# Kernel optimization log

Hardware: AMD Instinct MI355X
Metric: run time of the kernel (lower is better)

## Reference

```python
import jax, jax.numpy as jnp
import numpy as np

NS, NV = 16, 4            # multiplicities of 0e and 1o in in/out irreps
N_NODES, N_EDGES = 50000, 800000
INV_SQRT3 = 1.0 / np.sqrt(3.0).astype(np.float32)  # CG norm for 1o x 1o -> 0e
INV_SQRT2 = 1.0 / np.sqrt(2.0).astype(np.float32)  # 2 paths per output irrep
INV_SQRT_NS = 1.0 / np.sqrt(float(NS))
INV_SQRT_NV = 1.0 / np.sqrt(float(NV))


def setup_inputs() -> dict:
    key = jax.random.key(0)
    ks = jax.random.split(key, 8)
    node_attr = jax.random.normal(ks[0], (N_NODES, NS + 3 * NV), dtype=jnp.float32)
    edge_attr = jax.random.normal(ks[1], (N_EDGES, 64), dtype=jnp.float32)
    edge_sh = jax.random.normal(ks[2], (N_EDGES, 4), dtype=jnp.float32)
    edge_index = jax.random.randint(ks[3], (2, N_EDGES), 0, N_NODES, dtype=jnp.int32)
    n_weights = NS * NS + NV * NS + NS * NV + NV * NV  # 400
    W1 = jax.random.normal(ks[4], (64, 64), dtype=jnp.float32) / np.sqrt(64.0)
    b1 = jnp.zeros((64,), jnp.float32)
    W2 = jax.random.normal(ks[5], (64, n_weights), dtype=jnp.float32) / np.sqrt(64.0)
    b2 = jnp.zeros((n_weights,), jnp.float32)
    return {"node_attr": node_attr, "edge_attr": edge_attr, "edge_sh": edge_sh,
            "edge_index": edge_index, "W1": W1, "b1": b1, "W2": W2, "b2": b2}


def reference(node_attr, edge_attr, edge_sh, edge_index, W1, b1, W2, b2):
    E = edge_attr.shape[0]
    N = node_attr.shape[0]
    edge_src, edge_dst = edge_index[0], edge_index[1]

    # per-edge tensor-product weights from the MLP (dropout disabled at inference)
    h = jax.nn.relu(edge_attr @ W1 + b1)
    dense = h @ W2 + b2  # [E, 400]
    i0 = NS * NS
    i1 = i0 + NV * NS
    i2 = i1 + NS * NV
    w_ss = dense[:, :i0].reshape(E, NS, NS)   # 0e x 0e -> 0e
    w_vs = dense[:, i0:i1].reshape(E, NV, NS)  # 1o x 1o -> 0e
    w_sv = dense[:, i1:i2].reshape(E, NS, NV)  # 0e x 1o -> 1o
    w_vv = dense[:, i2:].reshape(E, NV, NV)    # 1o x 0e -> 1o

    # gather destination-node features per edge
    x = node_attr[edge_dst]            # [E, 28]
    x_s = x[:, :NS]                    # [E, NS]   scalars
    x_v = x[:, NS:].reshape(E, NV, 3)  # [E, NV,3] vectors
    sh_s = edge_sh[:, 0:1]             # [E, 1]
    sh_v = edge_sh[:, 1:4]             # [E, 3]

    # scalar outputs: two parity-allowed CG paths
    dot_vv = jnp.einsum('evd,ed->ev', x_v, sh_v) * INV_SQRT3  # 1o x 1o -> 0e
    out_s = (jnp.einsum('ei,eio->eo', x_s * sh_s, w_ss) * INV_SQRT_NS
             + jnp.einsum('ev,evo->eo', dot_vv, w_vs) * INV_SQRT_NV) * INV_SQRT2

    # vector outputs: two parity-allowed CG paths
    out_v = (jnp.einsum('ei,eio,ed->eod', x_s, w_sv, sh_v) * INV_SQRT_NS
             + jnp.einsum('evd,evo->eod', x_v * sh_s[:, :, None], w_vv) * INV_SQRT_NV) * INV_SQRT2

    out_e = jnp.concatenate([out_s, out_v.reshape(E, 3 * NV)], axis=-1)  # [E, 28]

    # scatter-mean onto source nodes
    summed = jax.ops.segment_sum(out_e, edge_src, num_segments=N)
    cnt = jax.ops.segment_sum(jnp.ones((E,), out_e.dtype), edge_src, num_segments=N)
    out = summed / jnp.maximum(cnt, 1.0)[:, None]

    # residual (out dim == in dim, so pad width is zero)
    return out + node_attr
```

## Files before the change

kernel.cpp:

```cpp
#include <hip/hip_runtime.h>

#define EDGES 800000
#define NODES 50000
#define CH 28
#define NWT 400
#define SCAN_NB 196
#define FIXS 65536.0f
#define FIXR (1.0f/65536.0f)

typedef __attribute__((ext_vector_type(8))) short bf16x8;
typedef __attribute__((ext_vector_type(4))) float f32x4;

#define WAVE_FENCE() __builtin_amdgcn_sched_barrier(0)

__device__ __forceinline__ short f2bf(float f) {
    union { float f; unsigned u; } v; v.f = f;
    unsigned r = v.u + 0x7FFFu + ((v.u >> 16) & 1u);
    return (short)(r >> 16);
}

#define SWZ(b, row) ((b) ^ (((row) & 7) << 4))

__global__ __launch_bounds__(256) void hist_kernel(const int* __restrict__ eidx,
                                                   int* __restrict__ counts) {
    int e = blockIdx.x * 256 + threadIdx.x;
    if (e < EDGES) atomicAdd(&counts[eidx[e]], 1);
}

__global__ __launch_bounds__(256) void scan1_kernel(const int* __restrict__ counts,
                                                    int* __restrict__ offsets,
                                                    int* __restrict__ bsum) {
    __shared__ int tmp[256];
    int t = threadIdx.x;
    int i = blockIdx.x * 256 + t;
    int v = (i < NODES) ? counts[i] : 0;
    tmp[t] = v;
    __syncthreads();
    int x = v;
    for (int d = 1; d < 256; d <<= 1) {
        int y = (t >= d) ? tmp[t - d] : 0;
        __syncthreads();
        x += y; tmp[t] = x;
        __syncthreads();
    }
    if (i < NODES) offsets[i] = x - v;
    if (t == 255) bsum[blockIdx.x] = x;
}

__global__ __launch_bounds__(256) void scan2_kernel(int* __restrict__ bsum) {
    __shared__ int tmp[256];
    int t = threadIdx.x;
    int v = (t < SCAN_NB) ? bsum[t] : 0;
    tmp[t] = v;
    __syncthreads();
    int x = v;
    for (int d = 1; d < 256; d <<= 1) {
        int y = (t >= d) ? tmp[t - d] : 0;
        __syncthreads();
        x += y; tmp[t] = x;
        __syncthreads();
    }
    if (t < SCAN_NB) bsum[t] = x - v;
}

__global__ __launch_bounds__(256) void scan3_kernel(int* __restrict__ offsets,
                                                    const int* __restrict__ bsum) {
    int i = blockIdx.x * 256 + threadIdx.x;
    if (i < NODES) offsets[i] += bsum[blockIdx.x];
}

__global__ __launch_bounds__(256) void perm_kernel(const int* __restrict__ eidx,
                                                   const int* __restrict__ offsets,
                                                   int* __restrict__ cursor,
                                                   int* __restrict__ perm) {
    int e = blockIdx.x * 256 + threadIdx.x;
    if (e < EDGES) {
        int s = eidx[e];
        int pos = offsets[s] + atomicAdd(&cursor[s], 1);
        perm[pos] = e;
    }
}

__global__ __launch_bounds__(256, 2) void tpconv_kernel(
    const float* __restrict__ node_attr,
    const float* __restrict__ edge_attr,
    const float* __restrict__ edge_sh,
    const int*   __restrict__ eidx,
    const float* __restrict__ W1,
    const float* __restrict__ b1,
    const float* __restrict__ W2,
    const float* __restrict__ b2,
    int* __restrict__ outq,
    const int* __restrict__ perm)
{
    __shared__ __align__(16) short w2t[NWT * 64];
    __shared__ float b2s[NWT];
    __shared__ __align__(16) short hbuf[4][16 * 64];
    __shared__ float edata[4][16 * 53];
    __shared__ int   srcb[4][16];
    __shared__ int   eids[4][16];

    const int tid  = threadIdx.x;
    const int lane = tid & 63;
    const int wid  = tid >> 6;
    const int cl   = lane & 15;
    const int qd   = lane >> 4;

    for (int f = tid; f < NWT * 64; f += 256) {
        int n = f >> 6, j = f & 63;
        int byte = SWZ(n * 128 + j * 2, n);
        w2t[byte >> 1] = f2bf(W2[j * NWT + n]);
    }
    for (int f = tid; f < NWT; f += 256) b2s[f] = b2[f];

    float b1v[4];
    bf16x8 w1f[2][4];
    #pragma unroll
    for (int nt = 0; nt < 4; ++nt) {
        b1v[nt] = b1[nt * 16 + cl];
        #pragma unroll
        for (int ks = 0; ks < 2; ++ks) {
            bf16x8 fr;
            #pragma unroll
            for (int i = 0; i < 8; ++i) {
                int k = ks * 32 + qd * 8 + i;
                fr[i] = f2bf(W1[k * 64 + nt * 16 + cl]);
            }
            w1f[ks][nt] = fr;
        }
    }
    __syncthreads();

    const float INV3 = 0.57735026919f;
    const float CS_  = 0.17677669529f;
    const float CV_  = 0.35355339059f;

    const int tiles = EDGES / 16;
    for (int tile = blockIdx.x * 4 + wid; tile < tiles; tile += gridDim.x * 4) {
        const int ebase = tile * 16;

        if (lane < 16) {
            const int slot = ebase + lane;
            const int e  = perm[slot];
            const int s  = eidx[e];
            const int dn = eidx[EDGES + e];
            srcb[wid][lane] = s;
            eids[wid][lane] = e;
            const float4 sh4 = *reinterpret_cast<const float4*>(edge_sh + (size_t)e * 4);
            float xs[16], xv[12];
            {
                const float4* xp = reinterpret_cast<const float4*>(node_attr + (size_t)dn * CH);
                float4 q0 = xp[0], q1 = xp[1], q2 = xp[2], q3 = xp[3], q4 = xp[4], q5 = xp[5], q6 = xp[6];
                xs[0]=q0.x; xs[1]=q0.y; xs[2]=q0.z; xs[3]=q0.w;
                xs[4]=q1.x; xs[5]=q1.y; xs[6]=q1.z; xs[7]=q1.w;
                xs[8]=q2.x; xs[9]=q2.y; xs[10]=q2.z; xs[11]=q2.w;
                xs[12]=q3.x; xs[13]=q3.y; xs[14]=q3.z; xs[15]=q3.w;
                xv[0]=q4.x; xv[1]=q4.y; xv[2]=q4.z; xv[3]=q4.w;
                xv[4]=q5.x; xv[5]=q5.y; xv[6]=q5.z; xv[7]=q5.w;
                xv[8]=q6.x; xv[9]=q6.y; xv[10]=q6.z; xv[11]=q6.w;
            }
            const float shs = sh4.x, sv0 = sh4.y, sv1 = sh4.z, sv2 = sh4.w;
            float* ed = &edata[wid][lane * 53];
            #pragma unroll
            for (int i = 0; i < 16; ++i) {
                ed[i]      = xs[i] * shs * CS_;
                ed[20 + i] = xs[i] * CS_;
            }
            #pragma unroll
            for (int v = 0; v < 4; ++v) {
                float dot = (xv[3*v] * sv0 + xv[3*v+1] * sv1 + xv[3*v+2] * sv2) * INV3;
                ed[16 + v] = dot * CV_;
                ed[36 + 3*v + 0] = xv[3*v + 0] * shs * CV_;
                ed[36 + 3*v + 1] = xv[3*v + 1] * shs * CV_;
                ed[36 + 3*v + 2] = xv[3*v + 2] * shs * CV_;
            }
            ed[48] = sv0; ed[49] = sv1; ed[50] = sv2;
        }
        WAVE_FENCE();

        const int es = eids[wid][cl];
        const float4* ap = reinterpret_cast<const float4*>(edge_attr + (size_t)es * 64);
        float4 a0 = ap[qd*2], a1 = ap[qd*2 + 1], a2 = ap[8 + qd*2], a3 = ap[8 + qd*2 + 1];
        bf16x8 af0, af1;
        af0[0]=f2bf(a0.x); af0[1]=f2bf(a0.y); af0[2]=f2bf(a0.z); af0[3]=f2bf(a0.w);
        af0[4]=f2bf(a1.x); af0[5]=f2bf(a1.y); af0[6]=f2bf(a1.z); af0[7]=f2bf(a1.w);
        af1[0]=f2bf(a2.x); af1[1]=f2bf(a2.y); af1[2]=f2bf(a2.z); af1[3]=f2bf(a2.w);
        af1[4]=f2bf(a3.x); af1[5]=f2bf(a3.y); af1[6]=f2bf(a3.z); af1[7]=f2bf(a3.w);

        short* hb = hbuf[wid];
        #pragma unroll
        for (int nt = 0; nt < 4; ++nt) {
            f32x4 acc = { b1v[nt], b1v[nt], b1v[nt], b1v[nt] };
            acc = __builtin_amdgcn_mfma_f32_16x16x32_bf16(af0, w1f[0][nt], acc, 0, 0, 0);
            acc = __builtin_amdgcn_mfma_f32_16x16x32_bf16(af1, w1f[1][nt], acc, 0, 0, 0);
            #pragma unroll
            for (int r = 0; r < 4; ++r) {
                int m = qd * 4 + r;
                float hv = fmaxf(acc[r], 0.0f);
                int byte = SWZ(m * 128 + (nt * 16 + cl) * 2, m);
                hb[byte >> 1] = f2bf(hv);
            }
        }
        WAVE_FENCE();

        bf16x8 h0 = *reinterpret_cast<bf16x8*>(reinterpret_cast<char*>(hb) + SWZ(cl * 128 + qd * 16, cl));
        bf16x8 h1 = *reinterpret_cast<bf16x8*>(reinterpret_cast<char*>(hb) + SWZ(cl * 128 + 64 + qd * 16, cl));
        WAVE_FENCE();

        f32x4 outs = {0.f, 0.f, 0.f, 0.f};
        f32x4 pacc = {0.f, 0.f, 0.f, 0.f};
        float qacc[4][3] = {{0,0,0},{0,0,0},{0,0,0},{0,0,0}};
        const float* edw = edata[wid];
        const char* wb = reinterpret_cast<const char*>(w2t);
        #pragma unroll
        for (int ct = 0; ct < 25; ++ct) {
            int n = ct * 16 + cl;
            bf16x8 bf0 = *reinterpret_cast<const bf16x8*>(wb + SWZ(n * 128 + qd * 16, n));
            bf16x8 bf1 = *reinterpret_cast<const bf16x8*>(wb + SWZ(n * 128 + 64 + qd * 16, n));
            float bb = b2s[n];
            f32x4 t = { bb, bb, bb, bb };
            t = __builtin_amdgcn_mfma_f32_16x16x32_bf16(h0, bf0, t, 0, 0, 0);
            t = __builtin_amdgcn_mfma_f32_16x16x32_bf16(h1, bf1, t, 0, 0, 0);
            if (ct < 16) {
                #pragma unroll
                for (int r = 0; r < 4; ++r)
                    outs[r] += edw[(qd*4 + r) * 53 + ct] * t[r];
            } else if (ct < 20) {
                #pragma unroll
                for (int r = 0; r < 4; ++r)
                    outs[r] += edw[(qd*4 + r) * 53 + 16 + (ct - 16)] * t[r];
            } else if (ct < 24) {
                int il = cl >> 2;
                #pragma unroll
                for (int r = 0; r < 4; ++r)
                    pacc[r] += edw[(qd*4 + r) * 53 + 20 + 4*(ct - 20) + il] * t[r];
            } else {
                int v = cl >> 2;
                #pragma unroll
                for (int r = 0; r < 4; ++r) {
                    #pragma unroll
                    for (int d = 0; d < 3; ++d)
                        qacc[r][d] += edw[(qd*4 + r) * 53 + 36 + 3*v + d] * t[r];
                }
            }
        }

        #pragma unroll
        for (int r = 0; r < 4; ++r) {
            float p = pacc[r];
            p += __shfl_xor(p, 4);
            p += __shfl_xor(p, 8);
            pacc[r] = p;
            #pragma unroll
            for (int d = 0; d < 3; ++d) {
                float q = qacc[r][d];
                q += __shfl_xor(q, 4);
                q += __shfl_xor(q, 8);
                qacc[r][d] = q;
            }
        }

        float* stf = reinterpret_cast<float*>(hb);
        #pragma unroll
        for (int r = 0; r < 4; ++r)
            stf[(qd*4 + r) * CH + cl] = outs[r];
        if (cl < 12) {
            int o = cl & 3, d = cl >> 2;
            #pragma unroll
            for (int r = 0; r < 4; ++r) {
                int m = qd * 4 + r;
                float qv = (d == 0) ? qacc[r][0] : ((d == 1) ? qacc[r][1] : qacc[r][2]);
                stf[m * CH + 16 + o * 3 + d] = edw[m * 53 + 48 + d] * pacc[r] + qv;
            }
        }
        WAVE_FENCE();

        if (lane < CH) {
            int cur = srcb[wid][0];
            float acc2 = 0.0f;
            for (int m = 0; m < 16; ++m) {
                int s = srcb[wid][m];
                if (s != cur) {
                    atomicAdd(&outq[(size_t)cur * CH + lane], (int)rintf(acc2 * FIXS));
                    acc2 = 0.0f; cur = s;
                }
                acc2 += stf[m * CH + lane];
            }
            atomicAdd(&outq[(size_t)cur * CH + lane], (int)rintf(acc2 * FIXS));
        }
        WAVE_FENCE();
    }
}

__global__ __launch_bounds__(256) void finalize_kernel(int* __restrict__ outq,
                                                       const int* __restrict__ counts,
                                                       const float* __restrict__ node_attr) {
    int idx = blockIdx.x * 256 + threadIdx.x;
    if (idx < NODES * CH) {
        int n = idx / CH;
        int q = outq[idx];
        float r = ((float)q * FIXR) / fmaxf((float)counts[n], 1.0f) + node_attr[idx];
        outq[idx] = __float_as_int(r);
    }
}

extern "C" void kernel_launch(void* const* d_in, const int* in_sizes, int n_in,
                              void* d_out, int out_size, void* d_ws, size_t ws_size,
                              hipStream_t stream) {
    const float* node_attr = (const float*)d_in[0];
    const float* edge_attr = (const float*)d_in[1];
    const float* edge_sh   = (const float*)d_in[2];
    const int*   eidx      = (const int*)d_in[3];
    const float* W1 = (const float*)d_in[4];
    const float* b1 = (const float*)d_in[5];
    const float* W2 = (const float*)d_in[6];
    const float* b2 = (const float*)d_in[7];

    const size_t OFF_OFFSETS = 204800;
    const size_t OFF_CURSOR  = 409600;
    const size_t OFF_BSUM    = 614400;
    const size_t OFF_PERM    = 616448;

    int* counts  = (int*)d_ws;
    int* offsets = (int*)((char*)d_ws + OFF_OFFSETS);
    int* cursor  = (int*)((char*)d_ws + OFF_CURSOR);
    int* bsum    = (int*)((char*)d_ws + OFF_BSUM);
    int* perm    = (int*)((char*)d_ws + OFF_PERM);

    const int EB = (EDGES + 255) / 256;

    hipMemsetAsync(counts, 0, NODES * sizeof(int), stream);
    hipMemsetAsync(cursor, 0, NODES * sizeof(int), stream);
    hipMemsetAsync(d_out, 0, (size_t)NODES * CH * sizeof(float), stream);

    hist_kernel<<<EB, 256, 0, stream>>>(eidx, counts);
    scan1_kernel<<<SCAN_NB, 256, 0, stream>>>(counts, offsets, bsum);
    scan2_kernel<<<1, 256, 0, stream>>>(bsum);
    scan3_kernel<<<SCAN_NB, 256, 0, stream>>>(offsets, bsum);
    perm_kernel<<<EB, 256, 0, stream>>>(eidx, offsets, cursor, perm);

    tpconv_kernel<<<512, 256, 0, stream>>>(node_attr, edge_attr, edge_sh, eidx,
                                           W1, b1, W2, b2, (int*)d_out, perm);
    finalize_kernel<<<(NODES * CH + 255) / 256, 256, 0, stream>>>((int*)d_out, counts, node_attr);
}
```

Measured before the change: 272.2 us.

## Software-pipeline per-tile gathers with register prefetch of next tile

Restructures the persistent tile loop so each wave prefetches the next tile's edge ids, edge_attr, edge_sh and node features into registers while it computes the current tile, and loads the perm index two tiles ahead. The node feature gather is split across 32 lanes instead of 16, and the shared eids buffer is removed. The aim is to hide global gather latency behind MFMA work, at the cost of more live registers under the 2-blocks-per-SM launch bound.

```diff
diff --git a/kernel.cpp b/kernel.cpp
--- a/kernel.cpp
+++ b/kernel.cpp
@@ -17,6 +17,13 @@
     union { float f; unsigned u; } v; v.f = f;
     unsigned r = v.u + 0x7FFFu + ((v.u >> 16) & 1u);
     return (short)(r >> 16);
+}
+
+__device__ __forceinline__ bf16x8 pack8(float4 u, float4 v) {
+    bf16x8 h;
+    h[0] = f2bf(u.x); h[1] = f2bf(u.y); h[2] = f2bf(u.z); h[3] = f2bf(u.w);
+    h[4] = f2bf(v.x); h[5] = f2bf(v.y); h[6] = f2bf(v.z); h[7] = f2bf(v.w);
+    return h;
 }
 
 #define SWZ(b, row) ((b) ^ (((row) & 7) << 4))
@@ -80,6 +87,13 @@
         perm[pos] = e;
     }
 }
+
+struct TileRegs {
+    float4 a0, a1, a2, a3;
+    float4 sh;
+    float4 x0, x1, x2, x3;
+    int es, src;
+};
 
 __global__ __launch_bounds__(256, 2) void tpconv_kernel(
     const float* __restrict__ node_attr,
@@ -98,7 +112,6 @@
     __shared__ __align__(16) short hbuf[4][16 * 64];
     __shared__ float edata[4][16 * 53];
     __shared__ int   srcb[4][16];
-    __shared__ int   eids[4][16];
 
     const int tid  = threadIdx.x;
     const int lane = tid & 63;
@@ -135,73 +148,101 @@
     const float CS_  = 0.17677669529f;
     const float CV_  = 0.35355339059f;
 
-    const int tiles = EDGES / 16;
-    for (int tile = blockIdx.x * 4 + wid; tile < tiles; tile += gridDim.x * 4) {
-        const int ebase = tile * 16;
-
-        if (lane < 16) {
-            const int slot = ebase + lane;
-            const int e  = perm[slot];
-            const int s  = eidx[e];
-            const int dn = eidx[EDGES + e];
-            srcb[wid][lane] = s;
-            eids[wid][lane] = e;
-            const float4 sh4 = *reinterpret_cast<const float4*>(edge_sh + (size_t)e * 4);
-            float xs[16], xv[12];
-            {
-                const float4* xp = reinterpret_cast<const float4*>(node_attr + (size_t)dn * CH);
-                float4 q0 = xp[0], q1 = xp[1], q2 = xp[2], q3 = xp[3], q4 = xp[4], q5 = xp[5], q6 = xp[6];
-                xs[0]=q0.x; xs[1]=q0.y; xs[2]=q0.z; xs[3]=q0.w;
-                xs[4]=q1.x; xs[5]=q1.y; xs[6]=q1.z; xs[7]=q1.w;
-                xs[8]=q2.x; xs[9]=q2.y; xs[10]=q2.z; xs[11]=q2.w;
-                xs[12]=q3.x; xs[13]=q3.y; xs[14]=q3.z; xs[15]=q3.w;
-                xv[0]=q4.x; xv[1]=q4.y; xv[2]=q4.z; xv[3]=q4.w;
-                xv[4]=q5.x; xv[5]=q5.y; xv[6]=q5.z; xv[7]=q5.w;
-                xv[8]=q6.x; xv[9]=q6.y; xv[10]=q6.z; xv[11]=q6.w;
-            }
-            const float shs = sh4.x, sv0 = sh4.y, sv1 = sh4.z, sv2 = sh4.w;
-            float* ed = &edata[wid][lane * 53];
+    const int tiles  = EDGES / 16;
+    const int STRIDE = gridDim.x << 2;
+    const int w0     = blockIdx.x * 4 + wid;
+
+    short* hb  = hbuf[wid];
+    float* edwv = edata[wid];
+    const char* wb = reinterpret_cast<const char*>(w2t);
+
+    TileRegs C, N;
+    {
+        int slot = w0 * 16 + cl;
+        C.es  = perm[slot];
+        C.src = eidx[C.es];
+        int dst = eidx[EDGES + C.es];
+        const float4* ap = reinterpret_cast<const float4*>(edge_attr + (size_t)C.es * 64);
+        C.a0 = ap[qd*2]; C.a1 = ap[qd*2+1]; C.a2 = ap[8+qd*2]; C.a3 = ap[8+qd*2+1];
+        C.sh = *reinterpret_cast<const float4*>(edge_sh + (size_t)C.es * 4);
+        if (lane < 32) {
+            const float4* xp = reinterpret_cast<const float4*>(node_attr + (size_t)dst * CH);
+            if (lane < 16) { C.x0 = xp[0]; C.x1 = xp[1]; C.x2 = xp[2]; C.x3 = xp[3]; }
+            else           { C.x0 = xp[4]; C.x1 = xp[5]; C.x2 = xp[6]; }
+        }
+        int t1 = w0 + STRIDE;
+        int slot1 = (t1 < tiles) ? t1 * 16 + cl : cl;
+        N.es = perm[slot1];
+    }
+
+    for (int t = w0; t < tiles; t += STRIDE) {
+        int t2 = t + 2 * STRIDE;
+        int slot2 = (t2 < tiles) ? t2 * 16 + cl : cl;
+        int esF = perm[slot2];
+
+        N.src = eidx[N.es];
+        int ndst = eidx[EDGES + N.es];
+        {
+            const float4* ap = reinterpret_cast<const float4*>(edge_attr + (size_t)N.es * 64);
+            N.a0 = ap[qd*2]; N.a1 = ap[qd*2+1]; N.a2 = ap[8+qd*2]; N.a3 = ap[8+qd*2+1];
+            N.sh = *reinterpret_cast<const float4*>(edge_sh + (size_t)N.es * 4);
+        }
+
+        {
+            const float shs = C.sh.x, sv0 = C.sh.y, sv1 = C.sh.z, sv2 = C.sh.w;
+            float* ed = &edwv[cl * 53];
+            if (lane < 16) {
+                srcb[wid][cl] = C.src;
+                float xs[16] = { C.x0.x, C.x0.y, C.x0.z, C.x0.w,
+                                 C.x1.x, C.x1.y, C.x1.z, C.x1.w,
+                                 C.x2.x, C.x2.y, C.x2.z, C.x2.w,
+                                 C.x3.x, C.x3.y, C.x3.z, C.x3.w };
+                #pragma unroll
+                for (int i = 0; i < 16; ++i) {
+                    ed[i]      = xs[i] * shs * CS_;
+                    ed[20 + i] = xs[i] * CS_;
+                }
+            } else if (lane < 32) {
+                float xv[12] = { C.x0.x, C.x0.y, C.x0.z, C.x0.w,
+                                 C.x1.x, C.x1.y, C.x1.z, C.x1.w,
+                                 C.x2.x, C.x2.y, C.x2.z, C.x2.w };
+                #pragma unroll
+                for (int v = 0; v < 4; ++v) {
+                    float dot = (xv[3*v] * sv0 + xv[3*v+1] * sv1 + xv[3*v+2] * sv2) * INV3;
+                    ed[16 + v] = dot * CV_;
+                    ed[36 + 3*v + 0] = xv[3*v + 0] * shs * CV_;
+                    ed[36 + 3*v + 1] = xv[3*v + 1] * shs * CV_;
+                    ed[36 + 3*v + 2] = xv[3*v + 2] * shs * CV_;
+                }
+                ed[48] = sv0; ed[49] = sv1; ed[50] = sv2;
+            }
+        }
+        WAVE_FENCE();
+
+        {
+            bf16x8 af0 = pack8(C.a0, C.a1);
+            bf16x8 af1 = pack8(C.a2, C.a3);
             #pragma unroll
-            for (int i = 0; i < 16; ++i) {
-                ed[i]      = xs[i] * shs * CS_;
-                ed[20 + i] = xs[i] * CS_;
-            }
-            #pragma unroll
-            for (int v = 0; v < 4; ++v) {
-                float dot = (xv[3*v] * sv0 + xv[3*v+1] * sv1 + xv[3*v+2] * sv2) * INV3;
-                ed[16 + v] = dot * CV_;
-                ed[36 + 3*v + 0] = xv[3*v + 0] * shs * CV_;
-                ed[36 + 3*v + 1] = xv[3*v + 1] * shs * CV_;
-                ed[36 + 3*v + 2] = xv[3*v + 2] * shs * CV_;
-            }
-            ed[48] = sv0; ed[49] = sv1; ed[50] = sv2;
-        }
-        WAVE_FENCE();
-
-        const int es = eids[wid][cl];
-        const float4* ap = reinterpret_cast<const float4*>(edge_attr + (size_t)es * 64);
-        float4 a0 = ap[qd*2], a1 = ap[qd*2 + 1], a2 = ap[8 + qd*2], a3 = ap[8 + qd*2 + 1];
-        bf16x8 af0, af1;
-        af0[0]=f2bf(a0.x); af0[1]=f2bf(a0.y); af0[2]=f2bf(a0.z); af0[3]=f2bf(a0.w);
-        af0[4]=f2bf(a1.x); af0[5]=f2bf(a1.y); af0[6]=f2bf(a1.z); af0[7]=f2bf(a1.w);
-        af1[0]=f2bf(a2.x); af1[1]=f2bf(a2.y); af1[2]=f2bf(a2.z); af1[3]=f2bf(a2.w);
-        af1[4]=f2bf(a3.x); af1[5]=f2bf(a3.y); af1[6]=f2bf(a3.z); af1[7]=f2bf(a3.w);
-
-        short* hb = hbuf[wid];
-        #pragma unroll
-        for (int nt = 0; nt < 4; ++nt) {
-            f32x4 acc = { b1v[nt], b1v[nt], b1v[nt], b1v[nt] };
-            acc = __builtin_amdgcn_mfma_f32_16x16x32_bf16(af0, w1f[0][nt], acc, 0, 0, 0);
-            acc = __builtin_amdgcn_mfma_f32_16x16x32_bf16(af1, w1f[1][nt], acc, 0, 0, 0);
-            #pragma unroll
-            for (int r = 0; r < 4; ++r) {
-                int m = qd * 4 + r;
-                float hv = fmaxf(acc[r], 0.0f);
-                int byte = SWZ(m * 128 + (nt * 16 + cl) * 2, m);
-                hb[byte >> 1] = f2bf(hv);
-            }
-        }
-        WAVE_FENCE();
+            for (int nt = 0; nt < 4; ++nt) {
+                f32x4 acc = { b1v[nt], b1v[nt], b1v[nt], b1v[nt] };
+                acc = __builtin_amdgcn_mfma_f32_16x16x32_bf16(af0, w1f[0][nt], acc, 0, 0, 0);
+                acc = __builtin_amdgcn_mfma_f32_16x16x32_bf16(af1, w1f[1][nt], acc, 0, 0, 0);
+                #pragma unroll
+                for (int r = 0; r < 4; ++r) {
+                    int m = qd * 4 + r;
+                    float hv = fmaxf(acc[r], 0.0f);
+                    int byte = SWZ(m * 128 + (nt * 16 + cl) * 2, m);
+                    hb[byte >> 1] = f2bf(hv);
+                }
+            }
+        }
+        WAVE_FENCE();
+
+        if (lane < 32) {
+            const float4* xp = reinterpret_cast<const float4*>(node_attr + (size_t)ndst * CH);
+            if (lane < 16) { N.x0 = xp[0]; N.x1 = xp[1]; N.x2 = xp[2]; N.x3 = xp[3]; }
+            else           { N.x0 = xp[4]; N.x1 = xp[5]; N.x2 = xp[6]; }
+        }
 
         bf16x8 h0 = *reinterpret_cast<bf16x8*>(reinterpret_cast<char*>(hb) + SWZ(cl * 128 + qd * 16, cl));
         bf16x8 h1 = *reinterpret_cast<bf16x8*>(reinterpret_cast<char*>(hb) + SWZ(cl * 128 + 64 + qd * 16, cl));
@@ -210,37 +251,36 @@
         f32x4 outs = {0.f, 0.f, 0.f, 0.f};
         f32x4 pacc = {0.f, 0.f, 0.f, 0.f};
         float qacc[4][3] = {{0,0,0},{0,0,0},{0,0,0},{0,0,0}};
-        const float* edw = edata[wid];
-        const char* wb = reinterpret_cast<const char*>(w2t);
+        const float* edw = edwv;
         #pragma unroll
         for (int ct = 0; ct < 25; ++ct) {
             int n = ct * 16 + cl;
             bf16x8 bf0 = *reinterpret_cast<const bf16x8*>(wb + SWZ(n * 128 + qd * 16, n));
             bf16x8 bf1 = *reinterpret_cast<const bf16x8*>(wb + SWZ(n * 128 + 64 + qd * 16, n));
             float bb = b2s[n];
-            f32x4 t = { bb, bb, bb, bb };
-            t = __builtin_amdgcn_mfma_f32_16x16x32_bf16(h0, bf0, t, 0, 0, 0);
-            t = __builtin_amdgcn_mfma_f32_16x16x32_bf16(h1, bf1, t, 0, 0, 0);
+            f32x4 tt = { bb, bb, bb, bb };
+            tt = __builtin_amdgcn_mfma_f32_16x16x32_bf16(h0, bf0, tt, 0, 0, 0);
+            tt = __builtin_amdgcn_mfma_f32_16x16x32_bf16(h1, bf1, tt, 0, 0, 0);
             if (ct < 16) {
                 #pragma unroll
                 for (int r = 0; r < 4; ++r)
-                    outs[r] += edw[(qd*4 + r) * 53 + ct] * t[r];
+                    outs[r] += edw[(qd*4 + r) * 53 + ct] * tt[r];
             } else if (ct < 20) {
                 #pragma unroll
                 for (int r = 0; r < 4; ++r)
-                    outs[r] += edw[(qd*4 + r) * 53 + 16 + (ct - 16)] * t[r];
+                    outs[r] += edw[(qd*4 + r) * 53 + 16 + (ct - 16)] * tt[r];
             } else if (ct < 24) {
                 int il = cl >> 2;
                 #pragma unroll
                 for (int r = 0; r < 4; ++r)
-                    pacc[r] += edw[(qd*4 + r) * 53 + 20 + 4*(ct - 20) + il] * t[r];
+                    pacc[r] += edw[(qd*4 + r) * 53 + 20 + 4*(ct - 20) + il] * tt[r];
             } else {
                 int v = cl >> 2;
                 #pragma unroll
                 for (int r = 0; r < 4; ++r) {
                     #pragma unroll
                     for (int d = 0; d < 3; ++d)
-                        qacc[r][d] += edw[(qd*4 + r) * 53 + 36 + 3*v + d] * t[r];
+                        qacc[r][d] += edw[(qd*4 + r) * 53 + 36 + 3*v + d] * tt[r];
                 }
             }
         }
@@ -289,6 +329,9 @@
             atomicAdd(&outq[(size_t)cur * CH + lane], (int)rintf(acc2 * FIXS));
         }
         WAVE_FENCE();
+
+        C = N;
+        N.es = esF;
     }
 }
 
```

After: 270.2 us. No clear change (-0.7%).
